# Kernel tuning notes

Hardware: AMD Instinct MI355X
Metric: run time of the kernel (lower is better)

Reference implementation:

```python
import jax, jax.numpy as jnp
import numpy as np

N_HEAD, D_MODEL, D_K, D_V = 16, 1024, 64, 64
BN_EPS = 1e-5
NEG_INF = -1e9


def setup_inputs() -> dict:
    key = jax.random.key(0)
    ks = jax.random.split(key, 10)
    B, L = 4, 1024
    q = jax.random.normal(ks[0], (B, L, D_MODEL), dtype=jnp.float32)
    k = jax.random.normal(ks[1], (B, L, D_MODEL), dtype=jnp.float32)
    v = jax.random.normal(ks[2], (B, L, D_MODEL), dtype=jnp.float32)
    attn_mask = jax.random.randint(ks[3], (B, L, L), 0, 2) == 1  # True -> masked out
    s = 1.0 / np.sqrt(D_MODEL)
    w_qs = jax.random.normal(ks[4], (N_HEAD, D_MODEL, D_K), dtype=jnp.float32) * s
    w_ks = jax.random.normal(ks[5], (N_HEAD, D_MODEL, D_K), dtype=jnp.float32) * s
    w_vs = jax.random.normal(ks[6], (N_HEAD, D_MODEL, D_V), dtype=jnp.float32) * s
    proj_w = jax.random.normal(ks[7], (D_MODEL, N_HEAD * D_V), dtype=jnp.float32) * s
    proj_b = jnp.zeros((D_MODEL,), dtype=jnp.float32)
    bn_gamma = jnp.ones((D_MODEL,), dtype=jnp.float32)
    bn_beta = jnp.zeros((D_MODEL,), dtype=jnp.float32)
    return {"q": q, "k": k, "v": v, "attn_mask": attn_mask,
            "w_qs": w_qs, "w_ks": w_ks, "w_vs": w_vs,
            "proj_w": proj_w, "proj_b": proj_b,
            "bn_gamma": bn_gamma, "bn_beta": bn_beta}


def reference(q, k, v, attn_mask, w_qs, w_ks, w_vs, proj_w, proj_b, bn_gamma, bn_beta):
    B, Lq, D = q.shape
    temper = jnp.asarray(np.sqrt(D), dtype=q.dtype)
    residual = q
    # per-head projections: (H, B, L, dk)
    qh = jnp.einsum('bld,hdk->hblk', q, w_qs)
    kh = jnp.einsum('bld,hdk->hblk', k, w_ks)
    vh = jnp.einsum('bld,hdv->hblv', v, w_vs)
    # scaled dot-product attention, temper = sqrt(d_model)
    scores = jnp.einsum('hbqk,hbsk->hbqs', qh, kh) / temper
    scores = jnp.where(attn_mask[None], NEG_INF, scores)
    attns = jax.nn.softmax(scores, axis=-1)  # (H, B, Lq, Lk)
    out_h = jnp.einsum('hbqs,hbsv->hbqv', attns, vh)  # (H, B, Lq, dv)
    # concat heads along feature dim in head order
    out = jnp.transpose(out_h, (1, 2, 0, 3)).reshape(B, Lq, N_HEAD * D_V)
    out = out @ proj_w.T + proj_b
    # residual + BatchNorm1d over channel dim (batch stats, training-mode math)
    x = out + residual  # (B, L, D)
    mean = jnp.mean(x, axis=(0, 1))
    var = jnp.var(x, axis=(0, 1))
    x = (x - mean) * jax.lax.rsqrt(var + BN_EPS) * bn_gamma + bn_beta
    attns_flat = attns.reshape(N_HEAD * B, Lq, -1)
    return x, attns_flat
```

## Files before the change

kernel.cpp:

```cpp
#include <hip/hip_runtime.h>

typedef unsigned short ushort;
typedef __attribute__((ext_vector_type(4))) float floatx4;
typedef __bf16 bf16x8 __attribute__((ext_vector_type(8)));
typedef __bf16 bf16x4 __attribute__((ext_vector_type(4)));
typedef float f32x4 __attribute__((ext_vector_type(4)));

constexpr int NB = 4;
constexpr int NL = 1024;
constexpr int ND = 1024;
constexpr int NH = 16;
constexpr int NDK = 64;

#define QSCALE 0.045084230079650879f

union B4 { bf16x4 v; unsigned long long ll; };

__device__ __forceinline__ void st_bf(ushort* dst, float f){
  union { __bf16 h; ushort u; } z; z.h = (__bf16)f; *dst = z.u;
}

#define MFMA(a,b,c) __builtin_amdgcn_mfma_f32_16x16x32_bf16((a),(b),(c),0,0,0)

__global__ __launch_bounds__(256) void k_prep(const float* __restrict__ q,
                                              const float* __restrict__ k,
                                              const float* __restrict__ v,
                                              const float* __restrict__ pw,
                                              const float* __restrict__ w0,
                                              const float* __restrict__ w1,
                                              const float* __restrict__ w2,
                                              const int* __restrict__ M,
                                              ushort* __restrict__ qb,
                                              ushort* __restrict__ kb,
                                              ushort* __restrict__ vb,
                                              ushort* __restrict__ pwb,
                                              ushort* __restrict__ t0,
                                              ushort* __restrict__ t1,
                                              ushort* __restrict__ t2,
                                              unsigned long long* __restrict__ MB,
                                              float* __restrict__ part){
  __shared__ ushort T[64][65];
  const int bid = blockIdx.x;
  const int tid = threadIdx.x;

  if (bid < 6656){
    const int a = (bid < 2048) ? 0 : (bid < 4096) ? 1 : (bid < 6144) ? 2 : 3;
    const int rel = bid - a * 2048;
    const float* src = (a == 0) ? q : (a == 1) ? k : (a == 2) ? v : pw;
    ushort* dst = (a == 0) ? qb : (a == 1) ? kb : (a == 2) ? vb : pwb;
    const size_t base = ((size_t)rel * 256 + tid) * 8;
    floatx4 v0 = *(const floatx4*)(src + base);
    floatx4 v1 = *(const floatx4*)(src + base + 4);
    bf16x8 o;
    #pragma unroll
    for (int j = 0; j < 4; j++){ o[j] = (__bf16)v0[j]; o[4 + j] = (__bf16)v1[j]; }
    *(bf16x8*)(dst + base) = o;
    return;
  }
  if (bid < 7424){
    const int r = bid - 6656;
    const int z = r >> 8;
    const int h = (r >> 4) & 15, k0 = (r & 15) * 64;
    const float* src = (z == 0) ? w0 : (z == 1) ? w1 : w2;
    ushort* dst = (z == 0) ? t0 : (z == 1) ? t1 : t2;
    const int qd = tid >> 6, lo = tid & 63;
    #pragma unroll
    for (int i = 0; i < 16; i++){
      int kl = qd + i * 4;
      float f = src[((size_t)h * 1024 + k0 + kl) * 64 + lo];
      union { __bf16 h2; ushort u; } zz; zz.h2 = (__bf16)f;
      T[kl][lo] = zz.u;
    }
    __syncthreads();
    #pragma unroll
    for (int i = 0; i < 16; i++){
      int dk = qd + i * 4;
      dst[((size_t)h * 64 + dk) * 1024 + k0 + lo] = T[lo][dk];
    }
    return;
  }
  if (bid < 11520){
    const int r = bid - 7424;
    #pragma unroll
    for (int rep = 0; rep < 4; rep++){
      const int gid = r * 1024 + rep * 256 + tid;
      const int widx = gid >> 6;
      int m = M[(size_t)widx * 64 + (gid & 63)];
      unsigned long long bal = __ballot(m != 0);
      if ((gid & 63) == 0) MB[widx] = bal;
    }
    return;
  }
  *(floatx4*)(part + tid * 8) = f32x4{0.f, 0.f, 0.f, 0.f};
  *(floatx4*)(part + tid * 8 + 4) = f32x4{0.f, 0.f, 0.f, 0.f};
}

__global__ __launch_bounds__(256) void k_projm(const ushort* __restrict__ qbp,
                                               const ushort* __restrict__ kbp,
                                               const ushort* __restrict__ vbp,
                                               const ushort* __restrict__ wqT,
                                               const ushort* __restrict__ wkT,
                                               const ushort* __restrict__ wvT,
                                               ushort* __restrict__ qh,
                                               ushort* __restrict__ kh,
                                               ushort* __restrict__ vt){
  __shared__ bf16x8 Ach[8 * 128];
  __shared__ bf16x8 Bch[8 * 128];
  const int z = blockIdx.z;
  const ushort* Xb = (z == 0) ? qbp : (z == 1) ? kbp : vbp;
  const ushort* WT = (z == 0) ? wqT : (z == 1) ? wkT : wvT;
  const int tid = threadIdx.x;
  const int lane = tid & 63, wid = tid >> 6;
  const int g = lane >> 4, c = lane & 15;
  const int d = blockIdx.y * 8 + blockIdx.x;
  const int tile = (d & 7) * 32 + (d >> 3);
  const int row0 = (tile >> 3) * 128, col0 = (tile & 7) * 128;
  const int wm = (wid >> 1) * 64, wn = (wid & 1) * 64;

  f32x4 zero = {0.f, 0.f, 0.f, 0.f};
  f32x4 acc[4][4];
  #pragma unroll
  for (int i = 0; i < 4; i++)
    #pragma unroll
    for (int j = 0; j < 4; j++) acc[i][j] = zero;

  for (int k0 = 0; k0 < ND; k0 += 64){
    #pragma unroll
    for (int i = 0; i < 4; i++){
      int e = tid + i * 256;
      int kc = e & 7, m = e >> 3;
      Ach[kc * 128 + (m ^ kc)] = *(const bf16x8*)(Xb + (size_t)(row0 + m) * ND + k0 + kc * 8);
    }
    #pragma unroll
    for (int i = 0; i < 4; i++){
      int e = tid + i * 256;
      int kc = e & 7, n = e >> 3;
      int hh = (col0 + n) >> 6, dk = (col0 + n) & 63;
      Bch[kc * 128 + (n ^ kc)] = *(const bf16x8*)(WT + ((size_t)(hh << 6) + dk) * 1024 + k0 + kc * 8);
    }
    __syncthreads();
    bf16x8 bfr[4][2];
    #pragma unroll
    for (int ni = 0; ni < 4; ni++){
      int n = wn + ni * 16 + c;
      bfr[ni][0] = Bch[g * 128 + (n ^ g)];
      bfr[ni][1] = Bch[(4 + g) * 128 + (n ^ (4 + g))];
    }
    #pragma unroll
    for (int mi = 0; mi < 4; mi++){
      int m = wm + mi * 16 + c;
      bf16x8 a0 = Ach[g * 128 + (m ^ g)];
      bf16x8 a1 = Ach[(4 + g) * 128 + (m ^ (4 + g))];
      #pragma unroll
      for (int ni = 0; ni < 4; ni++){
        acc[mi][ni] = MFMA(a0, bfr[ni][0], acc[mi][ni]);
        acc[mi][ni] = MFMA(a1, bfr[ni][1], acc[mi][ni]);
      }
    }
    __syncthreads();
  }
  if (z == 2){
    #pragma unroll
    for (int mi = 0; mi < 4; mi++){
      #pragma unroll
      for (int ni = 0; ni < 4; ni++){
        int n = col0 + wn + ni * 16 + c;
        int hh = n >> 6, dk = n & 63;
        int m0 = row0 + wm + mi * 16 + g * 4;
        int bb = m0 >> 10, l = m0 & 1023;
        B4 o;
        #pragma unroll
        for (int r = 0; r < 4; r++) o.v[r] = (__bf16)acc[mi][ni][r];
        *(unsigned long long*)(vt + (((size_t)hh * NB + bb) * 64 + dk) * 1024 + l) = o.ll;
      }
    }
  } else {
    ushort* OUT = (z == 0) ? qh : kh;
    const float sc = (z == 0) ? QSCALE : 1.0f;
    #pragma unroll
    for (int mi = 0; mi < 4; mi++){
      #pragma unroll
      for (int ni = 0; ni < 4; ni++){
        #pragma unroll
        for (int r = 0; r < 4; r++){
          int m = row0 + wm + mi * 16 + g * 4 + r;
          int n = col0 + wn + ni * 16 + c;
          int bb = m >> 10, ls = m & 1023;
          int hh = n >> 6, dk = n & 63;
          st_bf(OUT + (((size_t)hh * NB + bb) * NL + ls) * NDK + dk, acc[mi][ni][r] * sc);
        }
      }
    }
  }
}

__global__ __launch_bounds__(256, 4) void k_attn(const ushort* __restrict__ QH,
                                                 const ushort* __restrict__ KH,
                                                 const ushort* __restrict__ VT,
                                                 const unsigned* __restrict__ MB,
                                                 float* __restrict__ ATT,
                                                 ushort* __restrict__ CTX){
  __shared__ bf16x8 Kch[512];
  __shared__ bf16x8 Vch[512];
  __shared__ ushort Ps[4][16][72];
  __shared__ unsigned Ms[64 * 33];
  const int tid = threadIdx.x;
  const int lane = tid & 63, wid = tid >> 6;
  const int g = lane >> 4, c = lane & 15;
  const int d = blockIdx.y * 16 + blockIdx.x;
  const int tile = (d & 7) * 128 + (d >> 3);
  const int hb = tile >> 4;
  const int q0 = (tile & 15) * 64;
  const int h = hb >> 2, b = hb & 3;

  const int q = q0 + wid * 16 + c;
  const size_t qkbase = (size_t)hb * NL;

  bf16x8 qf0 = *(const bf16x8*)(QH + (qkbase + q) * NDK + g * 8);
  bf16x8 qf1 = *(const bf16x8*)(QH + (qkbase + q) * NDK + 32 + g * 8);

  {
    const unsigned* mbase = MB + ((size_t)(b << 10) + q0) * 32;
    #pragma unroll
    for (int i = 0; i < 8; i++){
      int idx = tid + i * 256;
      int ql2 = idx >> 5, word = idx & 31;
      Ms[ql2 * 33 + word] = mbase[ql2 * 32 + word];
    }
  }
  const int ql = wid * 16 + c;
  const int mg = g * 4;

  const int i0 = tid * 2, i1 = tid * 2 + 1;
  const int sr0 = i0 >> 3, kc0 = i0 & 7;
  const int sr1 = i1 >> 3, kc1 = i1 & 7;
  const int vdv0 = tid >> 3, vkc0 = tid & 7;
  const int vdv1 = (tid + 256) >> 3, vkc1 = tid & 7;

  float rs = 0.f;
  bf16x8 kr0 = *(const bf16x8*)(KH + (qkbase + 0) * NDK + i0 * 8);
  bf16x8 kr1 = *(const bf16x8*)(KH + (qkbase + 0) * NDK + i1 * 8);
  for (int t = 0; t < 16; ++t){
    __syncthreads();
    Kch[sr0 * 8 + (kc0 ^ (sr0 & 7))] = kr0;
    Kch[sr1 * 8 + (kc1 ^ (sr1 & 7))] = kr1;
    __syncthreads();
    if (t < 15){
      const ushort* knext = KH + (qkbase + (t + 1) * 64) * NDK;
      kr0 = *(const bf16x8*)(knext + i0 * 8);
      kr1 = *(const bf16x8*)(knext + i1 * 8);
    }
    #pragma unroll
    for (int sub2 = 0; sub2 < 4; ++sub2){
      int s = sub2 * 16 + c;
      bf16x8 kf0 = Kch[s * 8 + (g ^ (s & 7))];
      bf16x8 kf1 = Kch[s * 8 + ((4 + g) ^ (s & 7))];
      f32x4 a = {0.f, 0.f, 0.f, 0.f};
      a = MFMA(kf0, qf0, a);
      a = MFMA(kf1, qf1, a);
      unsigned w = Ms[ql * 33 + t * 2 + (sub2 >> 1)];
      unsigned bits4 = (w >> (((sub2 & 1) << 4) + mg)) & 0xFu;
      #pragma unroll
      for (int r = 0; r < 4; r++)
        rs += ((bits4 >> r) & 1u) ? 0.f : __builtin_amdgcn_exp2f(a[r]);
    }
  }
  rs += __shfl_xor(rs, 16);
  rs += __shfl_xor(rs, 32);
  const float invd = 1.f / rs;

  f32x4 zero = {0.f, 0.f, 0.f, 0.f};
  f32x4 acc[4];
  #pragma unroll
  for (int i = 0; i < 4; i++) acc[i] = zero;

  kr0 = *(const bf16x8*)(KH + (qkbase + 0) * NDK + i0 * 8);
  kr1 = *(const bf16x8*)(KH + (qkbase + 0) * NDK + i1 * 8);
  bf16x8 vr0 = *(const bf16x8*)(VT + ((size_t)hb * 64 + vdv0) * 1024 + vkc0 * 8);
  bf16x8 vr1 = *(const bf16x8*)(VT + ((size_t)hb * 64 + vdv1) * 1024 + vkc1 * 8);

  for (int t = 0; t < 16; ++t){
    __syncthreads();
    Kch[sr0 * 8 + (kc0 ^ (sr0 & 7))] = kr0;
    Kch[sr1 * 8 + (kc1 ^ (sr1 & 7))] = kr1;
    Vch[vkc0 * 64 + (vdv0 ^ vkc0)] = vr0;
    Vch[vkc1 * 64 + (vdv1 ^ vkc1)] = vr1;
    __syncthreads();
    if (t < 15){
      const ushort* knext = KH + (qkbase + (t + 1) * 64) * NDK;
      kr0 = *(const bf16x8*)(knext + i0 * 8);
      kr1 = *(const bf16x8*)(knext + i1 * 8);
      const ushort* vnext = VT + (size_t)hb * 64 * 1024 + (t + 1) * 64;
      vr0 = *(const bf16x8*)(vnext + (size_t)vdv0 * 1024 + vkc0 * 8);
      vr1 = *(const bf16x8*)(vnext + (size_t)vdv1 * 1024 + vkc1 * 8);
    }
    #pragma unroll
    for (int sub2 = 0; sub2 < 4; ++sub2){
      int s = sub2 * 16 + c;
      bf16x8 kf0 = Kch[s * 8 + (g ^ (s & 7))];
      bf16x8 kf1 = Kch[s * 8 + ((4 + g) ^ (s & 7))];
      f32x4 a = {0.f, 0.f, 0.f, 0.f};
      a = MFMA(kf0, qf0, a);
      a = MFMA(kf1, qf1, a);
      unsigned w = Ms[ql * 33 + t * 2 + (sub2 >> 1)];
      unsigned bits4 = (w >> (((sub2 & 1) << 4) + mg)) & 0xFu;
      floatx4 pn;
      B4 pw;
      #pragma unroll
      for (int r = 0; r < 4; r++){
        float p = ((bits4 >> r) & 1u) ? 0.f : __builtin_amdgcn_exp2f(a[r]) * invd;
        pn[r] = p;
        pw.v[r] = (__bf16)p;
      }
      *(floatx4*)(ATT + ((size_t)hb * NL + q) * NL + (t * 4 + sub2) * 16 + g * 4) = pn;
      *(unsigned long long*)&Ps[wid][c][sub2 * 16 + g * 4] = pw.ll;
    }
    #pragma unroll
    for (int ss = 0; ss < 2; ++ss){
      bf16x8 afr = *(bf16x8*)&Ps[wid][c][ss * 32 + g * 8];
      #pragma unroll
      for (int ni = 0; ni < 4; ni++){
        int kcr = ss * 4 + g;
        bf16x8 vfr = Vch[kcr * 64 + ((ni * 16 + c) ^ kcr)];
        acc[ni] = MFMA(afr, vfr, acc[ni]);
      }
    }
  }

  #pragma unroll
  for (int ni = 0; ni < 4; ni++)
    #pragma unroll
    for (int r = 0; r < 4; r++){
      int qq = q0 + wid * 16 + g * 4 + r;
      int dv = ni * 16 + c;
      st_bf(CTX + ((size_t)b * NL + qq) * ND + h * NDK + dv, acc[ni][r]);
    }
}

__global__ __launch_bounds__(256) void k_projo(const ushort* __restrict__ CTX,
                                               const ushort* __restrict__ PWb,
                                               const float* __restrict__ PB,
                                               const float* __restrict__ RES,
                                               float* __restrict__ X,
                                               float* __restrict__ part){
  __shared__ bf16x8 Ach[8 * 128];
  __shared__ bf16x8 Bch[8 * 128];
  const int tid = threadIdx.x;
  const int lane = tid & 63, wid = tid >> 6;
  const int g = lane >> 4, c = lane & 15;
  const int d = blockIdx.y * 8 + blockIdx.x;
  const int tile = (d & 7) * 32 + (d >> 3);
  const int row0 = (tile >> 3) * 128, col0 = (tile & 7) * 128;
  const int wm = (wid >> 1) * 64, wn = (wid & 1) * 64;

  f32x4 zero = {0.f, 0.f, 0.f, 0.f};
  f32x4 acc[4][4];
  #pragma unroll
  for (int i = 0; i < 4; i++)
    #pragma unroll
    for (int j = 0; j < 4; j++) acc[i][j] = zero;

  for (int k0 = 0; k0 < ND; k0 += 64){
    #pragma unroll
    for (int i = 0; i < 4; i++){
      int e = tid + i * 256;
      int kc = e & 7, m = e >> 3;
      Ach[kc * 128 + (m ^ kc)] = *(const bf16x8*)(CTX + (size_t)(row0 + m) * ND + k0 + kc * 8);
    }
    #pragma unroll
    for (int i = 0; i < 4; i++){
      int e = tid + i * 256;
      int kc = e & 7, n = e >> 3;
      Bch[kc * 128 + (n ^ kc)] = *(const bf16x8*)(PWb + (size_t)(col0 + n) * 1024 + k0 + kc * 8);
    }
    __syncthreads();
    bf16x8 bfr[4][2];
    #pragma unroll
    for (int ni = 0; ni < 4; ni++){
      int n = wn + ni * 16 + c;
      bfr[ni][0] = Bch[g * 128 + (n ^ g)];
      bfr[ni][1] = Bch[(4 + g) * 128 + (n ^ (4 + g))];
    }
    #pragma unroll
    for (int mi = 0; mi < 4; mi++){
      int m = wm + mi * 16 + c;
      bf16x8 a0 = Ach[g * 128 + (m ^ g)];
      bf16x8 a1 = Ach[(4 + g) * 128 + (m ^ (4 + g))];
      #pragma unroll
      for (int ni = 0; ni < 4; ni++){
        acc[mi][ni] = MFMA(a0, bfr[ni][0], acc[mi][ni]);
        acc[mi][ni] = MFMA(a1, bfr[ni][1], acc[mi][ni]);
      }
    }
    __syncthreads();
  }
  float s_[4] = {0.f, 0.f, 0.f, 0.f}, s2_[4] = {0.f, 0.f, 0.f, 0.f};
  #pragma unroll
  for (int mi = 0; mi < 4; mi++)
    #pragma unroll
    for (int ni = 0; ni < 4; ni++)
      #pragma unroll
      for (int r = 0; r < 4; r++){
        int m = row0 + wm + mi * 16 + g * 4 + r;
        int n = col0 + wn + ni * 16 + c;
        float val = acc[mi][ni][r] + PB[n] + RES[(size_t)m * ND + n];
        X[(size_t)m * ND + n] = val;
        s_[ni] += val; s2_[ni] += val * val;
      }
  #pragma unroll
  for (int ni = 0; ni < 4; ni++){
    float a = s_[ni], b2 = s2_[ni];
    a += __shfl_xor(a, 16); b2 += __shfl_xor(b2, 16);
    a += __shfl_xor(a, 32); b2 += __shfl_xor(b2, 32);
    if (g == 0){
      int n = col0 + wn + ni * 16 + c;
      atomicAdd(&part[n], a);
      atomicAdd(&part[1024 + n], b2);
    }
  }
}

__global__ __launch_bounds__(256) void k_bnst2(const float* __restrict__ part,
                                               float* __restrict__ MV){
  const int cx = blockIdx.x * 256 + threadIdx.x;
  float s = part[cx], s2 = part[1024 + cx];
  float mean = s * (1.f / (NB * NL));
  float var = s2 * (1.f / (NB * NL)) - mean * mean;
  MV[cx] = mean;
  MV[ND + cx] = rsqrtf(var + 1e-5f);
}

__global__ __launch_bounds__(256) void k_bnapply(float* __restrict__ X,
                                                 const float* __restrict__ MV,
                                                 const float* __restrict__ G,
                                                 const float* __restrict__ Bt){
  const int idx = blockIdx.x * 256 + threadIdx.x;
  const size_t base = (size_t)idx * 8;
  const int d0 = (int)(base & (ND - 1));
  floatx4 x0 = *(const floatx4*)(X + base);
  floatx4 x1 = *(const floatx4*)(X + base + 4);
  floatx4 o0, o1;
  #pragma unroll
  for (int e = 0; e < 4; e++){
    int d = d0 + e;
    o0[e] = (x0[e] - MV[d]) * MV[ND + d] * G[d] + Bt[d];
    int d2 = d0 + 4 + e;
    o1[e] = (x1[e] - MV[d2]) * MV[ND + d2] * G[d2] + Bt[d2];
  }
  *(floatx4*)(X + base) = o0;
  *(floatx4*)(X + base + 4) = o1;
}

extern "C" void kernel_launch(void* const* d_in, const int* in_sizes, int n_in,
                              void* d_out, int out_size, void* d_ws, size_t ws_size,
                              hipStream_t stream){
  const float* q      = (const float*)d_in[0];
  const float* k      = (const float*)d_in[1];
  const float* v      = (const float*)d_in[2];
  const int*   mask   = (const int*)d_in[3];
  const float* w_qs   = (const float*)d_in[4];
  const float* w_ks   = (const float*)d_in[5];
  const float* w_vs   = (const float*)d_in[6];
  const float* proj_w = (const float*)d_in[7];
  const float* proj_b = (const float*)d_in[8];
  const float* gamma  = (const float*)d_in[9];
  const float* beta   = (const float*)d_in[10];

  float* out_x   = (float*)d_out;
  float* out_att = out_x + (size_t)NB * NL * ND;

  char* ws = (char*)d_ws;
  ushort* qb  = (ushort*)(ws);
  ushort* kb  = (ushort*)(ws + (8u  << 20));
  ushort* vb  = (ushort*)(ws + (16u << 20));
  ushort* qh  = (ushort*)(ws + (24u << 20));
  ushort* kh  = (ushort*)(ws + (32u << 20));
  ushort* vt  = (ushort*)(ws + (40u << 20));
  ushort* wqT = (ushort*)(ws + (48u << 20));
  ushort* wkT = (ushort*)(ws + (50u << 20));
  ushort* wvT = (ushort*)(ws + (52u << 20));
  ushort* pwb = (ushort*)(ws + (54u << 20));
  unsigned long long* mb = (unsigned long long*)(ws + (56u << 20));
  float*  part = (float*)(ws + (57u << 20));
  float*  mv   = (float*)(ws + (58u << 20));
  ushort* ctx  = qb;

  dim3 blk(256);
  k_prep<<<dim3(11521), blk, 0, stream>>>(q, k, v, proj_w, w_qs, w_ks, w_vs, mask,
                                          qb, kb, vb, pwb, wqT, wkT, wvT, mb, part);
  k_projm<<<dim3(8, 32, 3), blk, 0, stream>>>(qb, kb, vb, wqT, wkT, wvT, qh, kh, vt);
  k_attn<<<dim3(16, 64), blk, 0, stream>>>(qh, kh, vt, (const unsigned*)mb, out_att, ctx);
  k_projo<<<dim3(8, 32), blk, 0, stream>>>(ctx, pwb, proj_b, q, out_x, part);
  k_bnst2<<<dim3(4), blk, 0, stream>>>(part, mv);
  k_bnapply<<<dim3(NB * NL * ND / 8 / 256), blk, 0, stream>>>(out_x, mv, gamma, beta);
}
```

Measured before the change: 187.2 us.

## Fuse BatchNorm into output projection via grid barrier; fold softmax normalizer into MFMA bias

The separate BN-stats and BN-apply kernels are removed. The output projection kernel keeps its results in registers, waits at a global atomic-counter barrier until all 256 blocks have added their partial sums, then normalizes and writes X once. This avoids a full extra read and write of the 16 MB output plus two launches, but it relies on all 256 blocks being resident at the same time to avoid deadlock. In attention, the per-row 1/sum multiply is replaced by seeding the MFMA accumulator with -log2(sum), so exp2 gives normalized probabilities directly.

```diff
diff --git a/kernel.cpp b/kernel.cpp
--- a/kernel.cpp
+++ b/kernel.cpp
@@ -93,6 +93,7 @@
   }
   *(floatx4*)(part + tid * 8) = f32x4{0.f, 0.f, 0.f, 0.f};
   *(floatx4*)(part + tid * 8 + 4) = f32x4{0.f, 0.f, 0.f, 0.f};
+  if (tid == 0) *(unsigned*)(part + 2048) = 0u;
 }
 
 __global__ __launch_bounds__(256) void k_projm(const ushort* __restrict__ qbp,
@@ -267,12 +268,12 @@
   }
   rs += __shfl_xor(rs, 16);
   rs += __shfl_xor(rs, 32);
-  const float invd = 1.f / rs;
-
-  f32x4 zero = {0.f, 0.f, 0.f, 0.f};
+  const float lsh = -__log2f(rs);
+
   f32x4 acc[4];
   #pragma unroll
-  for (int i = 0; i < 4; i++) acc[i] = zero;
+  for (int i = 0; i < 4; i++) acc[i] = f32x4{0.f, 0.f, 0.f, 0.f};
+  const f32x4 cin = {lsh, lsh, lsh, lsh};
 
   kr0 = *(const bf16x8*)(KH + (qkbase + 0) * NDK + i0 * 8);
   kr1 = *(const bf16x8*)(KH + (qkbase + 0) * NDK + i1 * 8);
@@ -299,7 +300,7 @@
       int s = sub2 * 16 + c;
       bf16x8 kf0 = Kch[s * 8 + (g ^ (s & 7))];
       bf16x8 kf1 = Kch[s * 8 + ((4 + g) ^ (s & 7))];
-      f32x4 a = {0.f, 0.f, 0.f, 0.f};
+      f32x4 a = cin;
       a = MFMA(kf0, qf0, a);
       a = MFMA(kf1, qf1, a);
       unsigned w = Ms[ql * 33 + t * 2 + (sub2 >> 1)];
@@ -308,7 +309,7 @@
       B4 pw;
       #pragma unroll
       for (int r = 0; r < 4; r++){
-        float p = ((bits4 >> r) & 1u) ? 0.f : __builtin_amdgcn_exp2f(a[r]) * invd;
+        float p = ((bits4 >> r) & 1u) ? 0.f : __builtin_amdgcn_exp2f(a[r]);
         pn[r] = p;
         pw.v[r] = (__bf16)p;
       }
@@ -341,6 +342,8 @@
                                                const ushort* __restrict__ PWb,
                                                const float* __restrict__ PB,
                                                const float* __restrict__ RES,
+                                               const float* __restrict__ G,
+                                               const float* __restrict__ Bt,
                                                float* __restrict__ X,
                                                float* __restrict__ part){
   __shared__ bf16x8 Ach[8 * 128];
@@ -352,6 +355,7 @@
   const int tile = (d & 7) * 32 + (d >> 3);
   const int row0 = (tile >> 3) * 128, col0 = (tile & 7) * 128;
   const int wm = (wid >> 1) * 64, wn = (wid & 1) * 64;
+  unsigned* cnt = (unsigned*)(part + 2048);
 
   f32x4 zero = {0.f, 0.f, 0.f, 0.f};
   f32x4 acc[4][4];
@@ -404,7 +408,7 @@
         int m = row0 + wm + mi * 16 + g * 4 + r;
         int n = col0 + wn + ni * 16 + c;
         float val = acc[mi][ni][r] + PB[n] + RES[(size_t)m * ND + n];
-        X[(size_t)m * ND + n] = val;
+        acc[mi][ni][r] = val;
         s_[ni] += val; s2_[ni] += val * val;
       }
   #pragma unroll
@@ -418,37 +422,34 @@
       atomicAdd(&part[1024 + n], b2);
     }
   }
-}
-
-__global__ __launch_bounds__(256) void k_bnst2(const float* __restrict__ part,
-                                               float* __restrict__ MV){
-  const int cx = blockIdx.x * 256 + threadIdx.x;
-  float s = part[cx], s2 = part[1024 + cx];
-  float mean = s * (1.f / (NB * NL));
-  float var = s2 * (1.f / (NB * NL)) - mean * mean;
-  MV[cx] = mean;
-  MV[ND + cx] = rsqrtf(var + 1e-5f);
-}
-
-__global__ __launch_bounds__(256) void k_bnapply(float* __restrict__ X,
-                                                 const float* __restrict__ MV,
-                                                 const float* __restrict__ G,
-                                                 const float* __restrict__ Bt){
-  const int idx = blockIdx.x * 256 + threadIdx.x;
-  const size_t base = (size_t)idx * 8;
-  const int d0 = (int)(base & (ND - 1));
-  floatx4 x0 = *(const floatx4*)(X + base);
-  floatx4 x1 = *(const floatx4*)(X + base + 4);
-  floatx4 o0, o1;
-  #pragma unroll
-  for (int e = 0; e < 4; e++){
-    int d = d0 + e;
-    o0[e] = (x0[e] - MV[d]) * MV[ND + d] * G[d] + Bt[d];
-    int d2 = d0 + 4 + e;
-    o1[e] = (x1[e] - MV[d2]) * MV[ND + d2] * G[d2] + Bt[d2];
-  }
-  *(floatx4*)(X + base) = o0;
-  *(floatx4*)(X + base + 4) = o1;
+  __syncthreads();
+  if (tid == 0){
+    __threadfence();
+    atomicAdd(cnt, 1u);
+    while (__hip_atomic_load(cnt, __ATOMIC_ACQUIRE, __HIP_MEMORY_SCOPE_AGENT) < 256u)
+      __builtin_amdgcn_s_sleep(8);
+  }
+  __syncthreads();
+  __threadfence();
+  constexpr float invN = 1.f / (NB * NL);
+  #pragma unroll
+  for (int ni = 0; ni < 4; ni++){
+    int n = col0 + wn + ni * 16 + c;
+    float sm  = __hip_atomic_load(&part[n], __ATOMIC_RELAXED, __HIP_MEMORY_SCOPE_AGENT);
+    float s2m = __hip_atomic_load(&part[1024 + n], __ATOMIC_RELAXED, __HIP_MEMORY_SCOPE_AGENT);
+    float mean = sm * invN;
+    float var = s2m * invN - mean * mean;
+    float rstd = rsqrtf(var + 1e-5f);
+    float a1 = rstd * G[n];
+    float a0 = Bt[n] - mean * a1;
+    #pragma unroll
+    for (int mi = 0; mi < 4; mi++)
+      #pragma unroll
+      for (int r = 0; r < 4; r++){
+        int m = row0 + wm + mi * 16 + g * 4 + r;
+        X[(size_t)m * ND + n] = acc[mi][ni][r] * a1 + a0;
+      }
+  }
 }
 
 extern "C" void kernel_launch(void* const* d_in, const int* in_sizes, int n_in,
@@ -482,7 +483,6 @@
   ushort* pwb = (ushort*)(ws + (54u << 20));
   unsigned long long* mb = (unsigned long long*)(ws + (56u << 20));
   float*  part = (float*)(ws + (57u << 20));
-  float*  mv   = (float*)(ws + (58u << 20));
   ushort* ctx  = qb;
 
   dim3 blk(256);
@@ -490,7 +490,5 @@
                                           qb, kb, vb, pwb, wqT, wkT, wvT, mb, part);
   k_projm<<<dim3(8, 32, 3), blk, 0, stream>>>(qb, kb, vb, wqT, wkT, wvT, qh, kh, vt);
   k_attn<<<dim3(16, 64), blk, 0, stream>>>(qh, kh, vt, (const unsigned*)mb, out_att, ctx);
-  k_projo<<<dim3(8, 32), blk, 0, stream>>>(ctx, pwb, proj_b, q, out_x, part);
-  k_bnst2<<<dim3(4), blk, 0, stream>>>(part, mv);
-  k_bnapply<<<dim3(NB * NL * ND / 8 / 256), blk, 0, stream>>>(out_x, mv, gamma, beta);
-}
+  k_projo<<<dim3(8, 32), blk, 0, stream>>>(ctx, pwb, proj_b, q, gamma, beta, out_x, part);
+}
```

Result: slower. 206.8 us (+10.5%).
